# Performance work log

Hardware: AMD Instinct MI355X
Metric: run time of the kernel (lower is better)

The kernel has to match this reference:

```python
import jax, jax.numpy as jnp
import numpy as np


def setup_inputs() -> dict:
    key = jax.random.key(0)
    k1, k2, k3, k4 = jax.random.split(key, 4)
    B, T, S, D = 32, 512, 1024, 1024
    inp = jax.random.normal(k1, (B, T, D), dtype=jnp.float32)
    ctx = jax.random.normal(k2, (B, S, D), dtype=jnp.float32)
    W_in = jax.random.normal(k3, (D, D), dtype=jnp.float32) * (1.0 / np.sqrt(D))
    W_out = jax.random.normal(k4, (D, 2 * D), dtype=jnp.float32) * (1.0 / np.sqrt(2 * D))
    return {"input": inp, "context": ctx, "W_in": W_in, "W_out": W_out}


def reference(input, context, W_in, W_out):
    # GlobalAttention, attn_type='general', no mask, no coverage, tgt_len > 1.
    B, T, D = input.shape
    S = context.shape[1]
    # score: (W_in h_t) . h_s   -> [B, T, S]
    h_t = jnp.einsum('btd,ed->bte', input, W_in)           # linear_in (no bias)
    align = jnp.einsum('btd,bsd->bts', h_t, context)
    align_vectors = jax.nn.softmax(align, axis=-1)          # [B, T, S]
    # weighted sum of context
    c = jnp.einsum('bts,bsd->btd', align_vectors, context)  # [B, T, D]
    # concat [c, input] -> linear_out (no bias for 'general') -> tanh
    concat_c = jnp.concatenate([c, input], axis=-1)          # [B, T, 2D]
    attn_h = jnp.tanh(jnp.einsum('btf,df->btd', concat_c, W_out))
    # not one_step: transpose to [T, B, ...]
    attn_h = jnp.transpose(attn_h, (1, 0, 2))
    align_vectors = jnp.transpose(align_vectors, (1, 0, 2))
    return attn_h, align_vectors
```

## Files before the change

kernel.cpp:

```cpp
#include <hip/hip_runtime.h>
#include <hip/hip_bf16.h>


typedef short bf16x8 __attribute__((ext_vector_type(8)));
typedef float f32x4 __attribute__((ext_vector_type(4)));
typedef unsigned short us;

#define NB 32
#define NT_ 512
#define NS 1024
#define ND 1024

__device__ inline us f2bf(float x) {
  unsigned u = __float_as_uint(x);
  u += 0x7FFFu + ((u >> 16) & 1u);
  return (us)(u >> 16);
}
__device__ inline float bf2f(us h) { return __uint_as_float(((unsigned)h) << 16); }

__device__ inline void store_split(us* __restrict__ hi, us* __restrict__ lo, size_t idx, float v) {
  us h = f2bf(v);
  hi[idx] = h;
  lo[idx] = f2bf(v - bf2f(h));
}

__global__ void ga_split(const float* __restrict__ src, us* __restrict__ hi,
                         us* __restrict__ lo, long n) {
  long i0 = ((long)blockIdx.x * blockDim.x + threadIdx.x) * 4;
  long stride = (long)gridDim.x * blockDim.x * 4;
  for (long i = i0; i < n; i += stride) {
    float4 v = *reinterpret_cast<const float4*>(src + i);
    ushort4 h, l;
    h.x = f2bf(v.x); l.x = f2bf(v.x - bf2f(h.x));
    h.y = f2bf(v.y); l.y = f2bf(v.y - bf2f(h.y));
    h.z = f2bf(v.z); l.z = f2bf(v.z - bf2f(h.z));
    h.w = f2bf(v.w); l.w = f2bf(v.w - bf2f(h.w));
    *reinterpret_cast<ushort4*>(hi + i) = h;
    *reinterpret_cast<ushort4*>(lo + i) = l;
  }
}

__global__ void ga_cvt(const float* __restrict__ src, us* __restrict__ dst, long n) {
  long i0 = ((long)blockIdx.x * blockDim.x + threadIdx.x) * 4;
  long stride = (long)gridDim.x * blockDim.x * 4;
  for (long i = i0; i < n; i += stride) {
    float4 v = *reinterpret_cast<const float4*>(src + i);
    ushort4 h;
    h.x = f2bf(v.x); h.y = f2bf(v.y); h.z = f2bf(v.z); h.w = f2bf(v.w);
    *reinterpret_cast<ushort4*>(dst + i) = h;
  }
}

__global__ void ga_transpose_split(const float* __restrict__ ctx, us* __restrict__ tHi,
                                   us* __restrict__ tLo) {
  __shared__ float tile[64][65];
  int s0 = blockIdx.x << 6, d0 = blockIdx.y << 6, b = blockIdx.z;
  const float* src = ctx + (size_t)b * NS * ND;
  int tid = threadIdx.x;
#pragma unroll
  for (int i = 0; i < 16; ++i) {
    int lin = (i << 8) + tid;
    int r = lin >> 6, c = lin & 63;
    tile[r][c] = src[(size_t)(s0 + r) * ND + d0 + c];
  }
  __syncthreads();
  us* oH = tHi + (size_t)b * ND * NS;
  us* oL = tLo + (size_t)b * ND * NS;
#pragma unroll
  for (int i = 0; i < 16; ++i) {
    int lin = (i << 8) + tid;
    int dr = lin >> 6, sc = lin & 63;
    float v = tile[sc][dr];
    size_t o = (size_t)(d0 + dr) * NS + s0 + sc;
    us h = f2bf(v);
    oH[o] = h;
    oL[o] = f2bf(v - bf2f(h));
  }
}

__global__ __launch_bounds__(256) void ga_softmax(float* __restrict__ al,
                                                  us* __restrict__ pHi, us* __restrict__ pLo) {
  int row = blockIdx.x;
  int tid = threadIdx.x;
  float* p = al + (size_t)row * NS;
  float4 v = *reinterpret_cast<const float4*>(p + (tid << 2));
  float m = fmaxf(fmaxf(v.x, v.y), fmaxf(v.z, v.w));
#pragma unroll
  for (int off = 32; off; off >>= 1) m = fmaxf(m, __shfl_xor(m, off));
  __shared__ float rmax[4], rsum[4];
  int wv = tid >> 6, ln = tid & 63;
  if (ln == 0) rmax[wv] = m;
  __syncthreads();
  m = fmaxf(fmaxf(rmax[0], rmax[1]), fmaxf(rmax[2], rmax[3]));
  float4 e;
  e.x = __expf(v.x - m); e.y = __expf(v.y - m);
  e.z = __expf(v.z - m); e.w = __expf(v.w - m);
  float s = e.x + e.y + e.z + e.w;
#pragma unroll
  for (int off = 32; off; off >>= 1) s += __shfl_xor(s, off);
  if (ln == 0) rsum[wv] = s;
  __syncthreads();
  s = rsum[0] + rsum[1] + rsum[2] + rsum[3];
  float inv = 1.0f / s;
  e.x *= inv; e.y *= inv; e.z *= inv; e.w *= inv;
  *reinterpret_cast<float4*>(p + (tid << 2)) = e;
  int t = row >> 5, b = row & 31;
  size_t o = ((size_t)b * NT_ + t) * NS + (tid << 2);
  ushort4 h, l;
  h.x = f2bf(e.x); l.x = f2bf(e.x - bf2f(h.x));
  h.y = f2bf(e.y); l.y = f2bf(e.y - bf2f(h.y));
  h.z = f2bf(e.z); l.z = f2bf(e.z - bf2f(h.z));
  h.w = f2bf(e.w); l.w = f2bf(e.w - bf2f(h.w));
  *reinterpret_cast<ushort4*>(pHi + o) = h;
  *reinterpret_cast<ushort4*>(pLo + o) = l;
}

__device__ inline void gload16(const us* g, void* l) {
  __builtin_amdgcn_global_load_lds((const __attribute__((address_space(1))) unsigned int*)g,
                                   (__attribute__((address_space(3))) unsigned int*)l, 16, 0, 0);
}

__device__ inline f32x4 mfma16(bf16x8 a, bf16x8 b, f32x4 c) {
  return __builtin_amdgcn_mfma_f32_16x16x32_bf16(a, b, c, 0, 0, 0);
}


#define STAGE_A(tt, q) do {                                                        \
    const us *sah_, *sal_;                                                         \
    if constexpr (MODE == 3) {                                                     \
      if ((tt) < (NT >> 1)) { sah_ = pAh + (size_t)(tt) * 32;                      \
                              sal_ = pAl + (size_t)(tt) * 32; }                    \
      else { sah_ = pA2h + (size_t)((tt) - (NT >> 1)) * 32;                        \
             sal_ = pA2l + (size_t)((tt) - (NT >> 1)) * 32; }                      \
    } else { sah_ = pAh + (size_t)(tt) * 32; sal_ = pAl + (size_t)(tt) * 32; }     \
    long so_ = aoff0 + (long)(q) * 64 * lda;                                       \
    char* d_ = lb + (((tt) & 1) << 16) + ((q) << 13) + sdst;                       \
    gload16(sah_ + so_, d_);                                                       \
    gload16(sal_ + so_, d_ + 16384);                                               \
  } while (0)

#define STAGE_B(tt, q) do {                                                        \
    long so_ = boff0 + (long)(q) * 32 * ldb + (long)(tt) * 32;                     \
    char* d_ = lb + (((tt) & 1) << 16) + 32768 + ((q) << 13) + sdst;               \
    gload16(pBh + so_, d_);                                                        \
    if constexpr (MODE != 3) gload16(pBl + so_, d_ + 16384);                       \
  } while (0)

#define PHASE(QM, QN, STAGE, TAIL) do {                                            \
    const char* pA_ = lb + (cur << 16) + ((QM) << 13);                             \
    const char* pB_ = lb + (cur << 16) + 32768 + ((QN) << 13);                     \
    bf16x8 ah_[4], al_[4], bh_[2], bl_[2];                                         \
    _Pragma("unroll") for (int m = 0; m < 4; ++m) {                                \
      ah_[m] = *(const bf16x8*)(pA_ + arb + (m << 10));                            \
      al_[m] = *(const bf16x8*)(pA_ + 16384 + arb + (m << 10));                    \
    }                                                                              \
    _Pragma("unroll") for (int n = 0; n < 2; ++n) {                                \
      bh_[n] = *(const bf16x8*)(pB_ + brb + (n << 10));                            \
      if constexpr (MODE != 3)                                                     \
        bl_[n] = *(const bf16x8*)(pB_ + 16384 + brb + (n << 10));                  \
    }                                                                              \
    STAGE;                                                                         \
    __builtin_amdgcn_s_barrier();                                                  \
    __builtin_amdgcn_s_setprio(1);                                                 \
    _Pragma("unroll") for (int m = 0; m < 4; ++m)                                  \
    _Pragma("unroll") for (int n = 0; n < 2; ++n) {                                \
      f32x4& a_ = acc[(QM) * 4 + m][(QN) * 2 + n];                                 \
      a_ = mfma16(ah_[m], bh_[n], a_);                                             \
      if constexpr (MODE != 3) a_ = mfma16(ah_[m], bl_[n], a_);                    \
      a_ = mfma16(al_[m], bh_[n], a_);                                             \
    }                                                                              \
    __builtin_amdgcn_s_setprio(0);                                                 \
    TAIL;                                                                          \
    __builtin_amdgcn_s_barrier();                                                  \
  } while (0)

#define VM_STEADY do {                                                             \
    if constexpr (MODE == 3) asm volatile("s_waitcnt vmcnt(3)" ::: "memory");      \
    else asm volatile("s_waitcnt vmcnt(4)" ::: "memory");                          \
  } while (0)

template <int MODE>
__global__ __launch_bounds__(512, 2) void ga_gemm8(
    const us* __restrict__ Ahi, const us* __restrict__ Alo,
    const us* __restrict__ A2hi, const us* __restrict__ A2lo,
    const us* __restrict__ Bhi, const us* __restrict__ Blo,
    void* __restrict__ out0, void* __restrict__ out1,
    int K, int lda, int ldb, long astride, long bstride) {
  __shared__ __align__(16) char lds[131072];
  const int NT = K >> 5;
  const int tid = threadIdx.x;
  const int lane = tid & 63;
  const int wv = tid >> 6;
  const int wr = wv >> 2, wc = wv & 3;
  const int fr = lane & 15;
  const int blk0 = lane >> 4;
  const int bx = blockIdx.x, by = blockIdx.y, bz = blockIdx.z;
  const int rowA = bx << 8, colB = by << 8;

  const us* pAh = Ahi + (size_t)bz * astride + (size_t)rowA * lda;
  const us* pAl = Alo + (size_t)bz * astride + (size_t)rowA * lda;
  const us* pA2h = (MODE == 3) ? A2hi + (size_t)rowA * lda : nullptr;
  const us* pA2l = (MODE == 3) ? A2lo + (size_t)rowA * lda : nullptr;
  const us* pBh = Bhi + (size_t)bz * bstride + (size_t)colB * ldb;
  const us* pBl = (MODE == 3) ? nullptr : Blo + (size_t)bz * bstride + (size_t)colB * ldb;

  const int sprow = tid >> 2;
  const int sblkx = ((tid & 3) ^ ((sprow >> 1) & 3)) << 3;
  const long aoff0 = (long)((sprow >> 6) * 128 + (sprow & 63)) * lda + sblkx;
  const long boff0 = (long)((sprow >> 5) * 64 + (sprow & 31)) * ldb + sblkx;
  char* lb = lds;
  const int sdst = tid << 4;

  const int rdsw = (blk0 ^ ((fr >> 1) & 3)) << 4;
  const int arb = (wr << 12) + (fr << 6) + rdsw;
  const int brb = (wc << 11) + (fr << 6) + rdsw;

  f32x4 zero = {0.f, 0.f, 0.f, 0.f};
  f32x4 acc[8][4];
#pragma unroll
  for (int i = 0; i < 8; ++i)
#pragma unroll
    for (int k = 0; k < 4; ++k) acc[i][k] = zero;

  STAGE_A(0, 0); STAGE_B(0, 0); STAGE_A(0, 1); STAGE_B(0, 1);
  STAGE_A(1, 0); STAGE_B(1, 0);
  VM_STEADY;
  __builtin_amdgcn_s_barrier();

  int cur = 0;
  for (int t = 0; t < NT; ++t) {
    const bool s1 = (t + 1 < NT), s2 = (t + 2 < NT);
    PHASE(0, 0, { if (s1) STAGE_A(t + 1, 1); }, {});
    PHASE(0, 1, { if (s1) STAGE_B(t + 1, 1); }, {});
    PHASE(1, 0, { if (s2) STAGE_A(t + 2, 0); }, {});
    PHASE(1, 1, { if (s2) STAGE_B(t + 2, 0); },
          { if (s1) { if (s2) { VM_STEADY; }
                      else { asm volatile("s_waitcnt vmcnt(0)" ::: "memory"); } } });
    cur ^= 1;
  }

#pragma unroll
  for (int i = 0; i < 8; ++i)
#pragma unroll
    for (int k = 0; k < 4; ++k)
#pragma unroll
      for (int j = 0; j < 4; ++j) {
        int r = rowA + (wr << 7) + ((i >> 2) << 6) + ((i & 3) << 4) + ((lane >> 4) << 2) + j;
        int c = colB + (wc << 6) + ((k >> 1) << 5) + ((k & 1) << 4) + fr;
        float v = acc[i][k][j];
        if constexpr (MODE == 0) {
          store_split((us*)out0, (us*)out1, (size_t)r * 1024 + c, v);
        } else if constexpr (MODE == 1) {
          ((float*)out0)[((size_t)r * NB + bz) * NS + c] = v;
        } else if constexpr (MODE == 2) {
          store_split((us*)out0, (us*)out1, ((size_t)bz * 512 + r) * 1024 + c, v);
        } else {
          int bb = r >> 9, tt2 = r & 511;
          ((float*)out0)[((size_t)tt2 * NB + bb) * ND + c] = tanhf(v);
        }
      }
}

extern "C" void kernel_launch(void* const* d_in, const int* in_sizes, int n_in,
                              void* d_out, int out_size, void* d_ws, size_t ws_size,
                              hipStream_t stream) {
  (void)in_sizes; (void)n_in; (void)out_size; (void)ws_size;
  const float* inp = (const float*)d_in[0];
  const float* ctx = (const float*)d_in[1];
  const float* Win = (const float*)d_in[2];
  const float* Wout = (const float*)d_in[3];
  float* out = (float*)d_out;

  char* w = (char*)d_ws;
  us* ctx_hi  = (us*)(w + 0);
  us* c_hi    = (us*)(w + 0);
  us* c_lo    = (us*)(w + 33554432);
  us* ctx_lo  = (us*)(w + 67108864);
  us* p_hi    = (us*)(w + 67108864);
  us* p_lo    = (us*)(w + 100663296);
  us* in_hi   = (us*)(w + 134217728);
  us* in_lo   = (us*)(w + 167772160);
  us* h_hi    = (us*)(w + 201326592);
  us* h_lo    = (us*)(w + 234881024);
  us* ctxT_lo = (us*)(w + 201326592);
  us* win_hi  = (us*)(w + 268435456);
  us* win_lo  = (us*)(w + 270532608);
  us* wout_b  = (us*)(w + 272629760);

  us* ctxT_hi = (us*)d_out;
  float* alignOut = out + 16777216;

  ga_split<<<2048, 256, 0, stream>>>(inp, in_hi, in_lo, 16777216L);
  ga_split<<<2048, 256, 0, stream>>>(ctx, ctx_hi, ctx_lo, 33554432L);
  ga_split<<<512, 256, 0, stream>>>(Win, win_hi, win_lo, 1048576L);
  ga_cvt<<<512, 256, 0, stream>>>(Wout, wout_b, 2097152L);

  ga_gemm8<0><<<dim3(64, 4, 1), 512, 0, stream>>>(in_hi, in_lo, nullptr, nullptr,
                                                  win_hi, win_lo, h_hi, h_lo,
                                                  1024, 1024, 1024, 0L, 0L);
  ga_gemm8<1><<<dim3(2, 4, 32), 512, 0, stream>>>(h_hi, h_lo, nullptr, nullptr,
                                                  ctx_hi, ctx_lo, alignOut, nullptr,
                                                  1024, 1024, 1024, 524288L, 1048576L);
  ga_transpose_split<<<dim3(16, 16, 32), 256, 0, stream>>>(ctx, ctxT_hi, ctxT_lo);
  ga_softmax<<<16384, 256, 0, stream>>>(alignOut, p_hi, p_lo);
  ga_gemm8<2><<<dim3(2, 4, 32), 512, 0, stream>>>(p_hi, p_lo, nullptr, nullptr,
                                                  ctxT_hi, ctxT_lo, c_hi, c_lo,
                                                  1024, 1024, 1024, 524288L, 1048576L);
  ga_gemm8<3><<<dim3(64, 4, 1), 512, 0, stream>>>(c_hi, c_lo, in_hi, in_lo,
                                                  wout_b, nullptr, out, nullptr,
                                                  2048, 1024, 2048, 0L, 0L);
}
```

Measured before the change: 661.6 us.

## Restructure GEMM main loop into two half-phases with full-B staging per K-step

Replaces the four-quadrant phase schedule with two phases per K-tile, each covering one half of the A rows against all four B column fragments. All of the B tile is staged at once, and the MFMAs are grouped by hi/lo product instead of being interleaved. Shared memory shrinks when B is not split, and the LDS XOR swizzle is removed. The loop is peeled so the last tiles need no per-iteration conditionals. Removing the swizzle risks LDS bank conflicts, and the explicit lgkmcnt(0) wait before each MFMA block may serialise LDS reads with compute.

```diff
diff --git a/kernel.cpp b/kernel.cpp
--- a/kernel.cpp
+++ b/kernel.cpp
@@ -125,95 +125,91 @@
 }
 
 
-#define STAGE_A(tt, q) do {                                                        \
-    const us *sah_, *sal_;                                                         \
+#define STG_A(ST, H) do {                                                          \
+    int p_ = tid >> 2;                                                             \
+    long gr_ = (long)(((p_ >> 6) << 7) + ((H) << 6) + (p_ & 63));                  \
+    long sc_ = gr_ * lda + ((tid & 3) << 3) + (long)(ST) * 32;                     \
+    char* d_ = lb + (((ST) & 1) ? BUFSZ : 0) + ((H) << 13) + (tid << 4);           \
+    const us *ah_, *al_;                                                           \
     if constexpr (MODE == 3) {                                                     \
-      if ((tt) < (NT >> 1)) { sah_ = pAh + (size_t)(tt) * 32;                      \
-                              sal_ = pAl + (size_t)(tt) * 32; }                    \
-      else { sah_ = pA2h + (size_t)((tt) - (NT >> 1)) * 32;                        \
-             sal_ = pA2l + (size_t)((tt) - (NT >> 1)) * 32; }                      \
-    } else { sah_ = pAh + (size_t)(tt) * 32; sal_ = pAl + (size_t)(tt) * 32; }     \
-    long so_ = aoff0 + (long)(q) * 64 * lda;                                       \
-    char* d_ = lb + (((tt) & 1) << 16) + ((q) << 13) + sdst;                       \
-    gload16(sah_ + so_, d_);                                                       \
-    gload16(sal_ + so_, d_ + 16384);                                               \
+      if ((ST) < (NT >> 1)) { ah_ = pAh + sc_; al_ = pAl + sc_; }                  \
+      else { ah_ = pA2h + sc_ - 1024; al_ = pA2l + sc_ - 1024; }                   \
+    } else { ah_ = pAh + sc_; al_ = pAl + sc_; }                                   \
+    gload16(ah_, d_);                                                              \
+    gload16(al_, d_ + 16384);                                                      \
   } while (0)
 
-#define STAGE_B(tt, q) do {                                                        \
-    long so_ = boff0 + (long)(q) * 32 * ldb + (long)(tt) * 32;                     \
-    char* d_ = lb + (((tt) & 1) << 16) + 32768 + ((q) << 13) + sdst;               \
-    gload16(pBh + so_, d_);                                                        \
-    if constexpr (MODE != 3) gload16(pBl + so_, d_ + 16384);                       \
+#define STG_B(ST) do {                                                             \
+    _Pragma("unroll") for (int s_ = 0; s_ < 2; ++s_) {                             \
+      int c_ = tid + (s_ << 9);                                                    \
+      long sc_ = (long)(c_ >> 2) * ldb + ((c_ & 3) << 3) + (long)(ST) * 32;        \
+      char* d_ = lb + (((ST) & 1) ? BUFSZ : 0) + 32768 + (c_ << 4);                \
+      gload16(pBh + sc_, d_);                                                      \
+      if constexpr (SPLITB) gload16(pBl + sc_, d_ + 16384);                        \
+    }                                                                              \
   } while (0)
 
-#define PHASE(QM, QN, STAGE, TAIL) do {                                            \
-    const char* pA_ = lb + (cur << 16) + ((QM) << 13);                             \
-    const char* pB_ = lb + (cur << 16) + 32768 + ((QN) << 13);                     \
-    bf16x8 ah_[4], al_[4], bh_[2], bl_[2];                                         \
+#define PHASE(H, STAGES, TAIL) do {                                                \
+    const char* bp_ = lb + (cur ? BUFSZ : 0);                                      \
+    bf16x8 ah_[4], al_[4], bh_[4], bl_[4];                                         \
     _Pragma("unroll") for (int m = 0; m < 4; ++m) {                                \
-      ah_[m] = *(const bf16x8*)(pA_ + arb + (m << 10));                            \
-      al_[m] = *(const bf16x8*)(pA_ + 16384 + arb + (m << 10));                    \
+      ah_[m] = *(const bf16x8*)(bp_ + ((H) << 13) + aoff + (m << 10));             \
+      al_[m] = *(const bf16x8*)(bp_ + 16384 + ((H) << 13) + aoff + (m << 10));     \
     }                                                                              \
-    _Pragma("unroll") for (int n = 0; n < 2; ++n) {                                \
-      bh_[n] = *(const bf16x8*)(pB_ + brb + (n << 10));                            \
-      if constexpr (MODE != 3)                                                     \
-        bl_[n] = *(const bf16x8*)(pB_ + 16384 + brb + (n << 10));                  \
+    _Pragma("unroll") for (int n = 0; n < 4; ++n) {                                \
+      bh_[n] = *(const bf16x8*)(bp_ + 32768 + boff + (n << 10));                   \
+      if constexpr (SPLITB)                                                        \
+        bl_[n] = *(const bf16x8*)(bp_ + 49152 + boff + (n << 10));                 \
     }                                                                              \
-    STAGE;                                                                         \
+    STAGES;                                                                        \
     __builtin_amdgcn_s_barrier();                                                  \
+    asm volatile("s_waitcnt lgkmcnt(0)" ::: "memory");                             \
+    __builtin_amdgcn_sched_barrier(0);                                             \
     __builtin_amdgcn_s_setprio(1);                                                 \
     _Pragma("unroll") for (int m = 0; m < 4; ++m)                                  \
-    _Pragma("unroll") for (int n = 0; n < 2; ++n) {                                \
-      f32x4& a_ = acc[(QM) * 4 + m][(QN) * 2 + n];                                 \
-      a_ = mfma16(ah_[m], bh_[n], a_);                                             \
-      if constexpr (MODE != 3) a_ = mfma16(ah_[m], bl_[n], a_);                    \
-      a_ = mfma16(al_[m], bh_[n], a_);                                             \
-    }                                                                              \
+      _Pragma("unroll") for (int n = 0; n < 4; ++n)                                \
+        acc[(H) * 4 + m][n] = mfma16(ah_[m], bh_[n], acc[(H) * 4 + m][n]);         \
+    if constexpr (SPLITB)                                                          \
+      _Pragma("unroll") for (int m = 0; m < 4; ++m)                                \
+        _Pragma("unroll") for (int n = 0; n < 4; ++n)                              \
+          acc[(H) * 4 + m][n] = mfma16(ah_[m], bl_[n], acc[(H) * 4 + m][n]);       \
+    _Pragma("unroll") for (int m = 0; m < 4; ++m)                                  \
+      _Pragma("unroll") for (int n = 0; n < 4; ++n)                                \
+        acc[(H) * 4 + m][n] = mfma16(al_[m], bh_[n], acc[(H) * 4 + m][n]);         \
     __builtin_amdgcn_s_setprio(0);                                                 \
     TAIL;                                                                          \
     __builtin_amdgcn_s_barrier();                                                  \
   } while (0)
 
-#define VM_STEADY do {                                                             \
-    if constexpr (MODE == 3) asm volatile("s_waitcnt vmcnt(3)" ::: "memory");      \
-    else asm volatile("s_waitcnt vmcnt(4)" ::: "memory");                          \
-  } while (0)
-
 template <int MODE>
-__global__ __launch_bounds__(512, 2) void ga_gemm8(
+__global__ __launch_bounds__(512, 2) void ga_gmh(
     const us* __restrict__ Ahi, const us* __restrict__ Alo,
     const us* __restrict__ A2hi, const us* __restrict__ A2lo,
     const us* __restrict__ Bhi, const us* __restrict__ Blo,
     void* __restrict__ out0, void* __restrict__ out1,
     int K, int lda, int ldb, long astride, long bstride) {
-  __shared__ __align__(16) char lds[131072];
+  constexpr bool SPLITB = (MODE != 3);
+  constexpr int BUFSZ = SPLITB ? 65536 : 49152;
+  __shared__ __align__(16) char lds[2 * BUFSZ];
+  char* lb = lds;
   const int NT = K >> 5;
   const int tid = threadIdx.x;
   const int lane = tid & 63;
   const int wv = tid >> 6;
   const int wr = wv >> 2, wc = wv & 3;
   const int fr = lane & 15;
-  const int blk0 = lane >> 4;
-  const int bx = blockIdx.x, by = blockIdx.y, bz = blockIdx.z;
-  const int rowA = bx << 8, colB = by << 8;
+  const int rowA = blockIdx.x << 8, colB = blockIdx.y << 8;
+  const int bz = blockIdx.z;
 
   const us* pAh = Ahi + (size_t)bz * astride + (size_t)rowA * lda;
   const us* pAl = Alo + (size_t)bz * astride + (size_t)rowA * lda;
   const us* pA2h = (MODE == 3) ? A2hi + (size_t)rowA * lda : nullptr;
   const us* pA2l = (MODE == 3) ? A2lo + (size_t)rowA * lda : nullptr;
   const us* pBh = Bhi + (size_t)bz * bstride + (size_t)colB * ldb;
-  const us* pBl = (MODE == 3) ? nullptr : Blo + (size_t)bz * bstride + (size_t)colB * ldb;
-
-  const int sprow = tid >> 2;
-  const int sblkx = ((tid & 3) ^ ((sprow >> 1) & 3)) << 3;
-  const long aoff0 = (long)((sprow >> 6) * 128 + (sprow & 63)) * lda + sblkx;
-  const long boff0 = (long)((sprow >> 5) * 64 + (sprow & 31)) * ldb + sblkx;
-  char* lb = lds;
-  const int sdst = tid << 4;
-
-  const int rdsw = (blk0 ^ ((fr >> 1) & 3)) << 4;
-  const int arb = (wr << 12) + (fr << 6) + rdsw;
-  const int brb = (wc << 11) + (fr << 6) + rdsw;
+  const us* pBl = SPLITB ? Blo + (size_t)bz * bstride + (size_t)colB * ldb : nullptr;
+
+  const int aoff = (wr << 12) + (fr << 6) + ((lane >> 4) << 4);
+  const int boff = (wc << 12) + (fr << 6) + ((lane >> 4) << 4);
 
   f32x4 zero = {0.f, 0.f, 0.f, 0.f};
   f32x4 acc[8][4];
@@ -222,22 +218,22 @@
 #pragma unroll
     for (int k = 0; k < 4; ++k) acc[i][k] = zero;
 
-  STAGE_A(0, 0); STAGE_B(0, 0); STAGE_A(0, 1); STAGE_B(0, 1);
-  STAGE_A(1, 0); STAGE_B(1, 0);
-  VM_STEADY;
+  STG_A(0, 0); STG_A(0, 1); STG_B(0); STG_A(1, 0);
+  asm volatile("s_waitcnt vmcnt(2)" ::: "memory");
   __builtin_amdgcn_s_barrier();
 
   int cur = 0;
-  for (int t = 0; t < NT; ++t) {
-    const bool s1 = (t + 1 < NT), s2 = (t + 2 < NT);
-    PHASE(0, 0, { if (s1) STAGE_A(t + 1, 1); }, {});
-    PHASE(0, 1, { if (s1) STAGE_B(t + 1, 1); }, {});
-    PHASE(1, 0, { if (s2) STAGE_A(t + 2, 0); }, {});
-    PHASE(1, 1, { if (s2) STAGE_B(t + 2, 0); },
-          { if (s1) { if (s2) { VM_STEADY; }
-                      else { asm volatile("s_waitcnt vmcnt(0)" ::: "memory"); } } });
+  for (int t = 0; t < NT - 2; ++t) {
+    PHASE(0, { STG_B(t + 1); STG_A(t + 1, 1); }, {});
+    PHASE(1, { STG_A(t + 2, 0); },
+          { asm volatile("s_waitcnt vmcnt(2)" ::: "memory"); });
     cur ^= 1;
   }
+  PHASE(0, { STG_B(NT - 1); STG_A(NT - 1, 1); }, {});
+  PHASE(1, {}, { asm volatile("s_waitcnt vmcnt(0)" ::: "memory"); });
+  cur ^= 1;
+  PHASE(0, {}, {});
+  PHASE(1, {}, {});
 
 #pragma unroll
   for (int i = 0; i < 8; ++i)
@@ -246,7 +242,7 @@
 #pragma unroll
       for (int j = 0; j < 4; ++j) {
         int r = rowA + (wr << 7) + ((i >> 2) << 6) + ((i & 3) << 4) + ((lane >> 4) << 2) + j;
-        int c = colB + (wc << 6) + ((k >> 1) << 5) + ((k & 1) << 4) + fr;
+        int c = colB + (wc << 6) + (k << 4) + fr;
         float v = acc[i][k][j];
         if constexpr (MODE == 0) {
           store_split((us*)out0, (us*)out1, (size_t)r * 1024 + c, v);
@@ -295,18 +291,18 @@
   ga_split<<<512, 256, 0, stream>>>(Win, win_hi, win_lo, 1048576L);
   ga_cvt<<<512, 256, 0, stream>>>(Wout, wout_b, 2097152L);
 
-  ga_gemm8<0><<<dim3(64, 4, 1), 512, 0, stream>>>(in_hi, in_lo, nullptr, nullptr,
-                                                  win_hi, win_lo, h_hi, h_lo,
-                                                  1024, 1024, 1024, 0L, 0L);
-  ga_gemm8<1><<<dim3(2, 4, 32), 512, 0, stream>>>(h_hi, h_lo, nullptr, nullptr,
-                                                  ctx_hi, ctx_lo, alignOut, nullptr,
-                                                  1024, 1024, 1024, 524288L, 1048576L);
+  ga_gmh<0><<<dim3(64, 4, 1), 512, 0, stream>>>(in_hi, in_lo, nullptr, nullptr,
+                                                win_hi, win_lo, h_hi, h_lo,
+                                                1024, 1024, 1024, 0L, 0L);
+  ga_gmh<1><<<dim3(2, 4, 32), 512, 0, stream>>>(h_hi, h_lo, nullptr, nullptr,
+                                                ctx_hi, ctx_lo, alignOut, nullptr,
+                                                1024, 1024, 1024, 524288L, 1048576L);
   ga_transpose_split<<<dim3(16, 16, 32), 256, 0, stream>>>(ctx, ctxT_hi, ctxT_lo);
   ga_softmax<<<16384, 256, 0, stream>>>(alignOut, p_hi, p_lo);
-  ga_gemm8<2><<<dim3(2, 4, 32), 512, 0, stream>>>(p_hi, p_lo, nullptr, nullptr,
-                                                  ctxT_hi, ctxT_lo, c_hi, c_lo,
-                                                  1024, 1024, 1024, 524288L, 1048576L);
-  ga_gemm8<3><<<dim3(64, 4, 1), 512, 0, stream>>>(c_hi, c_lo, in_hi, in_lo,
-                                                  wout_b, nullptr, out, nullptr,
-                                                  2048, 1024, 2048, 0L, 0L);
-}
+  ga_gmh<2><<<dim3(2, 4, 32), 512, 0, stream>>>(p_hi, p_lo, nullptr, nullptr,
+                                                ctxT_hi, ctxT_lo, c_hi, c_lo,
+                                                1024, 1024, 1024, 524288L, 1048576L);
+  ga_gmh<3><<<dim3(64, 4, 1), 512, 0, stream>>>(c_hi, c_lo, in_hi, in_lo,
+                                                wout_b, nullptr, out, nullptr,
+                                                2048, 1024, 2048, 0L, 0L);
+}
```

New measurement: 677.0 us. 1.02x slower.
